# Kernel tuning notes

Measured on AMD Instinct MI355X. Metric: run time of the kernel, lower is better.

## Reference

```python
import jax, jax.numpy as jnp
import numpy as np

EPS = 1e-5
NEG_SLOPE = 0.2

def _bn(x, gamma, beta):
    # BatchNorm1d in training mode: stats over (batch, length) per channel. x: [B,C,N]
    m = jnp.mean(x, axis=(0, 2), keepdims=True)
    v = jnp.mean((x - m) ** 2, axis=(0, 2), keepdims=True)  # biased variance
    return (x - m) * jax.lax.rsqrt(v + EPS) * gamma[None, :, None] + beta[None, :, None]

def setup_inputs() -> dict:
    key = jax.random.key(0)
    ks = jax.random.split(key, 7)
    B, C, N, H = 32, 64, 2048, 128
    s = 1.0 / np.sqrt(C)
    return {
        "x": jax.random.normal(ks[0], (B, C, N), dtype=jnp.float32),
        "wq": jax.random.normal(ks[1], (C, C), dtype=jnp.float32) * s,
        "wk": jax.random.normal(ks[2], (C, C), dtype=jnp.float32) * s,
        "wv": jax.random.normal(ks[3], (C, C), dtype=jnp.float32) * s,
        "w_ff1": jax.random.normal(ks[4], (H, C), dtype=jnp.float32) * s,
        "w_ff2": jax.random.normal(ks[5], (C, H), dtype=jnp.float32) * (1.0 / np.sqrt(H)),
        "bn1_gamma": jnp.ones((C,), dtype=jnp.float32),
        "bn1_beta": jnp.zeros((C,), dtype=jnp.float32),
        "bn2_gamma": jnp.ones((C,), dtype=jnp.float32),
        "bn2_beta": jnp.zeros((C,), dtype=jnp.float32),
    }

def reference(x, wq, wk, wv, w_ff1, w_ff2, bn1_gamma, bn1_beta, bn2_gamma, bn2_beta):
    # x: [B, C, N]; 1x1 convs are per-point channel matmuls
    C = x.shape[1]
    q = jnp.einsum('oc,bcn->bno', wq, x)          # [B,N,C]
    k = jnp.einsum('oc,bcn->bon', wk, x)          # [B,C,N]
    v = jnp.einsum('oc,bcn->bno', wv, x)          # [B,N,C] (v^T)
    energy = jnp.einsum('bnc,bcm->bnm', q, k)     # [B,N,N]
    attention = jax.nn.softmax(energy / jnp.sqrt(jnp.float32(C)), axis=-1)
    x_r = jnp.einsum('bnm,bmc->bcn', attention, v)  # [B,C,N]
    h = _bn(x + x_r, bn1_gamma, bn1_beta)
    ff = jnp.einsum('hc,bcn->bhn', w_ff1, h)      # [B,H,N]
    ff = jnp.where(ff >= 0, ff, NEG_SLOPE * ff)   # LeakyReLU(0.2)
    ff = jnp.einsum('ch,bhn->bcn', w_ff2, ff)     # [B,C,N]
    return _bn(h + ff, bn2_gamma, bn2_beta)
```

## Files before the change

kernel.cpp:

```cpp
#include <hip/hip_runtime.h>

#define B_ 32
#define C_ 64
#define N_ 2048
#define H_ 128

typedef unsigned short u16;
typedef unsigned int u32;
typedef float f32x4 __attribute__((ext_vector_type(4)));
typedef __bf16 bf16x8 __attribute__((ext_vector_type(8)));
typedef __bf16 bf16x4 __attribute__((ext_vector_type(4)));
typedef unsigned short u16x4 __attribute__((ext_vector_type(4)));

#define MFMA(a, b, c) __builtin_amdgcn_mfma_f32_16x16x32_bf16(a, b, c, 0, 0, 0)
#define LOG2E 1.44269504088896f

__device__ __forceinline__ int swz(int row, int cb) { return row * 128 + (cb ^ ((row & 7) << 4)); }
__device__ __forceinline__ int swz256(int row, int cb) { return row * 256 + (cb ^ ((row & 7) << 4)); }

__device__ __forceinline__ float b2f(u16 v) {
    union { u32 u; float f; } x; x.u = ((u32)v) << 16; return x.f;
}

__device__ __forceinline__ bf16x8 cvt8(const float* p, float s) {
    f32x4 a = *(const f32x4*)p, b = *(const f32x4*)(p + 4);
    bf16x8 o;
    o[0] = (__bf16)(a[0] * s); o[1] = (__bf16)(a[1] * s);
    o[2] = (__bf16)(a[2] * s); o[3] = (__bf16)(a[3] * s);
    o[4] = (__bf16)(b[0] * s); o[5] = (__bf16)(b[1] * s);
    o[6] = (__bf16)(b[2] * s); o[7] = (__bf16)(b[3] * s);
    return o;
}

__global__ __launch_bounds__(256) void qkv_k(
    const float* __restrict__ x,
    const float* __restrict__ wq, const float* __restrict__ wk, const float* __restrict__ wv,
    const float* __restrict__ w1, const float* __restrict__ w2,
    u16* __restrict__ Qg, u16* __restrict__ Kg, u16* __restrict__ Vg,
    u16* __restrict__ w1b, u16* __restrict__ w2b)
{
    const int b = blockIdx.y, nt = blockIdx.x, t = threadIdx.x;
    const int lane = t & 63, wave = t >> 6, g = lane >> 4, r16 = lane & 15;
    __shared__ __align__(16) u16 xT[128 * 64];
    const int n0 = nt * 128;

    bf16x8 wqf[4][2], wkf[4][2], wvf[4][2];
#pragma unroll
    for (int jt = 0; jt < 4; ++jt)
#pragma unroll
        for (int kc = 0; kc < 2; ++kc) {
            const int ro = (r16 + 16 * jt) * 64 + 8 * g + 32 * kc;
            wqf[jt][kc] = cvt8(wq + ro, 0.125f * LOG2E);
            wkf[jt][kc] = cvt8(wk + ro, 1.0f);
            wvf[jt][kc] = cvt8(wv + ro, 1.0f);
        }

    {
        int c = t >> 5;
        const int nn = (t & 31) * 4;
#pragma unroll
        for (int pass = 0; pass < 8; ++pass, c += 8) {
            f32x4 v = *(const f32x4*)&x[(size_t)(b * 64 + c) * 2048 + n0 + nn];
#pragma unroll
            for (int j = 0; j < 4; ++j)
                xT[swz(nn + j, 2 * c) >> 1] = __builtin_bit_cast(u16, (__bf16)v[j]);
        }
    }
    if (b == 0 && nt == 0) {
        for (int i = t; i < H_ * C_; i += 256) w1b[i] = __builtin_bit_cast(u16, (__bf16)w1[i]);
        for (int i = t; i < C_ * H_; i += 256) w2b[i] = __builtin_bit_cast(u16, (__bf16)w2[i]);
    }
    __syncthreads();

#pragma unroll
    for (int p = 0; p < 2; ++p) {
        const int nt16 = wave * 2 + p;
        bf16x8 xa[2];
#pragma unroll
        for (int kc = 0; kc < 2; ++kc)
            xa[kc] = *(const bf16x8*)&xT[swz(nt16 * 16 + r16, 16 * g + 64 * kc) >> 1];
#pragma unroll
        for (int jt = 0; jt < 4; ++jt) {
            f32x4 aq = {0.f, 0.f, 0.f, 0.f}, ak = {0.f, 0.f, 0.f, 0.f};
            aq = MFMA(wqf[jt][0], xa[0], aq); aq = MFMA(wqf[jt][1], xa[1], aq);
            ak = MFMA(wkf[jt][0], xa[0], ak); ak = MFMA(wkf[jt][1], xa[1], ak);
            bf16x4 qk, kk;
#pragma unroll
            for (int r = 0; r < 4; ++r) { qk[r] = (__bf16)aq[r]; kk[r] = (__bf16)ak[r]; }
            const size_t ro = (size_t)(b * 2048 + n0 + nt16 * 16 + r16) * 64 + 16 * jt + 4 * g;
            *(bf16x4*)&Qg[ro] = qk;
            *(bf16x4*)&Kg[ro] = kk;
        }
#pragma unroll
        for (int it = 0; it < 4; ++it) {
            f32x4 av = {0.f, 0.f, 0.f, 0.f};
            av = MFMA(xa[0], wvf[it][0], av);
            av = MFMA(xa[1], wvf[it][1], av);
            bf16x4 vk;
#pragma unroll
            for (int r = 0; r < 4; ++r) vk[r] = (__bf16)av[r];
            *(bf16x4*)&Vg[(size_t)(b * 64 + 16 * it + r16) * 2048 + n0 + nt16 * 16 + 4 * g] = vk;
        }
    }
}

__global__ __launch_bounds__(256) void attn_k(
    const u16* __restrict__ Qg, const u16* __restrict__ Kg, const u16* __restrict__ Vg,
    const float* __restrict__ x, u16* __restrict__ yb,
    float* __restrict__ ps, float* __restrict__ pq)
{
    const int t = threadIdx.x;
    const int lane = t & 63, wave = t >> 6, g = lane >> 4, r16 = lane & 15;
    const int L = blockIdx.x;
    const int xcd = L & 7, slot = L >> 3;
    const int b = xcd * 4 + (slot >> 4);
    const int qt = slot & 15;

    __shared__ __align__(16) u16 Lds16[24576];
    char* lds = (char*)Lds16;

    const int n0 = qt * 128 + wave * 32;
    bf16x8 qf[2][2];
#pragma unroll
    for (int u = 0; u < 2; ++u) {
        const u16* qrow = Qg + (size_t)(b * 2048 + n0 + 16 * u + r16) * 64 + 8 * g;
        qf[u][0] = *(const bf16x8*)qrow;
        qf[u][1] = *(const bf16x8*)(qrow + 32);
    }

    f32x4 acc[2][4];
    float m[2] = {-1e30f, -1e30f}, lp[2] = {0.f, 0.f};
#pragma unroll
    for (int u = 0; u < 2; ++u)
#pragma unroll
        for (int ct = 0; ct < 4; ++ct) acc[u][ct] = (f32x4){0.f, 0.f, 0.f, 0.f};

    const char* Kgb = (const char*)Kg + (size_t)b * 2048 * 128;
    const char* Vgb = (const char*)Vg + (size_t)b * 64 * 4096;
    const int srcxor = (((lane & 7) ^ (lane >> 3)) << 4);
    const int rowb = wave * 16 + (lane >> 3);

    int ka[8];
#pragma unroll
    for (int i = 0; i < 8; ++i)
        ka[i] = swz(16 * (i >> 1) + r16, 16 * g + 64 * (i & 1));
    const int pbase = 32768 + wave * 4096;
    int pw[2][4], pr[2][2];
#pragma unroll
    for (int u = 0; u < 2; ++u) {
#pragma unroll
        for (int it = 0; it < 4; ++it) pw[u][it] = pbase + u * 2048 + swz(r16, 32 * it + 8 * g);
#pragma unroll
        for (int kc = 0; kc < 2; ++kc) pr[u][kc] = pbase + u * 2048 + swz(r16, 16 * g + 64 * kc);
    }

    auto stage = [&](int kvt, int buf) {
#pragma unroll
        for (int j = 0; j < 2; ++j) {
            const char* gk = Kgb + (size_t)(kvt * 64 + rowb + 8 * j) * 128 + srcxor;
            const char* gv = Vgb + (size_t)(rowb + 8 * j) * 4096 + kvt * 128 + srcxor;
            char* lk = lds + buf * 8192 + (wave * 2 + j) * 1024;
            __builtin_amdgcn_global_load_lds(
                (const __attribute__((address_space(1))) void*)gk,
                (__attribute__((address_space(3))) void*)lk, 16, 0, 0);
            __builtin_amdgcn_global_load_lds(
                (const __attribute__((address_space(1))) void*)gv,
                (__attribute__((address_space(3))) void*)(lk + 16384), 16, 0, 0);
        }
    };

    auto tile = [&](int kvt, int buf) {
        __syncthreads();
        if (kvt + 1 < 32) stage(kvt + 1, buf ^ 1);
        const char* Kc = lds + buf * 8192;
        const char* Vc = Kc + 16384;

        bf16x8 kf[8];
#pragma unroll
        for (int i = 0; i < 8; ++i) kf[i] = *(const bf16x8*)(Kc + ka[i]);
        f32x4 s[2][4];
        __builtin_amdgcn_s_setprio(1);
#pragma unroll
        for (int it = 0; it < 4; ++it) {
            f32x4 a0 = {0.f, 0.f, 0.f, 0.f}, a1 = {0.f, 0.f, 0.f, 0.f};
            a0 = MFMA(kf[2 * it], qf[0][0], a0); a0 = MFMA(kf[2 * it + 1], qf[0][1], a0);
            a1 = MFMA(kf[2 * it], qf[1][0], a1); a1 = MFMA(kf[2 * it + 1], qf[1][1], a1);
            s[0][it] = a0; s[1][it] = a1;
        }
        __builtin_amdgcn_s_setprio(0);
        bf16x8 vf[8];
#pragma unroll
        for (int i = 0; i < 8; ++i) vf[i] = *(const bf16x8*)(Vc + ka[i]);

#pragma unroll
        for (int u = 0; u < 2; ++u) {
            float mi[4];
#pragma unroll
            for (int it = 0; it < 4; ++it)
                mi[it] = fmaxf(fmaxf(s[u][it][0], s[u][it][1]),
                               fmaxf(s[u][it][2], s[u][it][3]));
            float pm = fmaxf(fmaxf(mi[0], mi[1]), fmaxf(mi[2], mi[3]));
            pm = fmaxf(pm, __shfl_xor(pm, 16, 64));
            pm = fmaxf(pm, __shfl_xor(pm, 32, 64));
            if (!__all(pm <= m[u] + 8.f)) {
                const float mn = fmaxf(m[u], pm);
                const float al = exp2f(m[u] - mn);
                m[u] = mn; lp[u] *= al;
#pragma unroll
                for (int ct = 0; ct < 4; ++ct)
#pragma unroll
                    for (int r = 0; r < 4; ++r) acc[u][ct][r] *= al;
            }
            float ts[4];
#pragma unroll
            for (int it = 0; it < 4; ++it) {
                const float p0 = exp2f(s[u][it][0] - m[u]);
                const float p1 = exp2f(s[u][it][1] - m[u]);
                const float p2 = exp2f(s[u][it][2] - m[u]);
                const float p3 = exp2f(s[u][it][3] - m[u]);
                ts[it] = (p0 + p1) + (p2 + p3);
                bf16x4 pk;
                pk[0] = (__bf16)p0; pk[1] = (__bf16)p1;
                pk[2] = (__bf16)p2; pk[3] = (__bf16)p3;
                *(bf16x4*)(lds + pw[u][it]) = pk;
            }
            lp[u] += (ts[0] + ts[1]) + (ts[2] + ts[3]);
        }
        bf16x8 pf[2][2];
#pragma unroll
        for (int u = 0; u < 2; ++u) {
            pf[u][0] = *(const bf16x8*)(lds + pr[u][0]);
            pf[u][1] = *(const bf16x8*)(lds + pr[u][1]);
        }
        __builtin_amdgcn_s_setprio(1);
#pragma unroll
        for (int u = 0; u < 2; ++u)
#pragma unroll
            for (int ct = 0; ct < 4; ++ct) {
                acc[u][ct] = MFMA(vf[2 * ct], pf[u][0], acc[u][ct]);
                acc[u][ct] = MFMA(vf[2 * ct + 1], pf[u][1], acc[u][ct]);
            }
        __builtin_amdgcn_s_setprio(0);
    };

    stage(0, 0);
#pragma unroll 1
    for (int kvt = 0; kvt < 32; kvt += 2) {
        tile(kvt, 0);
        tile(kvt + 1, 1);
    }

    float sv[4][4], qv[4][4];
#pragma unroll
    for (int ct = 0; ct < 4; ++ct)
#pragma unroll
        for (int r = 0; r < 4; ++r) { sv[ct][r] = 0.f; qv[ct][r] = 0.f; }
#pragma unroll
    for (int u = 0; u < 2; ++u) {
        float l = lp[u];
        l += __shfl_xor(l, 16, 64);
        l += __shfl_xor(l, 32, 64);
        const float inv = 1.0f / l;
        const int n = n0 + 16 * u + r16;
#pragma unroll
        for (int ct = 0; ct < 4; ++ct) {
            bf16x4 ov;
#pragma unroll
            for (int r = 0; r < 4; ++r) {
                const int c = 16 * ct + 4 * g + r;
                const float o = acc[u][ct][r] * inv + x[(size_t)(b * 64 + c) * 2048 + n];
                sv[ct][r] += o;
                qv[ct][r] += o * o;
                ov[r] = (__bf16)o;
            }
            *(bf16x4*)&yb[(size_t)(b * 2048 + n) * 64 + 16 * ct + 4 * g] = ov;
        }
    }
#pragma unroll
    for (int d = 1; d <= 8; d <<= 1)
#pragma unroll
        for (int ct = 0; ct < 4; ++ct)
#pragma unroll
            for (int r = 0; r < 4; ++r) {
                sv[ct][r] += __shfl_xor(sv[ct][r], d, 64);
                qv[ct][r] += __shfl_xor(qv[ct][r], d, 64);
            }
    __syncthreads();
    float* sb = (float*)(lds + 32768);
    if (r16 == 0) {
#pragma unroll
        for (int ct = 0; ct < 4; ++ct)
#pragma unroll
            for (int r = 0; r < 4; ++r) {
                const int c = 16 * ct + 4 * g + r;
                sb[wave * 64 + c] = sv[ct][r];
                sb[256 + wave * 64 + c] = qv[ct][r];
            }
    }
    __syncthreads();
    if (t < 64) {
        ps[L * 64 + t] = sb[t] + sb[64 + t] + sb[128 + t] + sb[192 + t];
        pq[L * 64 + t] = sb[256 + t] + sb[320 + t] + sb[384 + t] + sb[448 + t];
    }
}

__global__ __launch_bounds__(256) void finalize_k(
    const float* __restrict__ psum, const float* __restrict__ psq,
    const float* __restrict__ gamma, const float* __restrict__ beta,
    float* __restrict__ ss, int nblk)
{
    const int c = blockIdx.x, t = threadIdx.x;
    const int lane = t & 63, wave = t >> 6;
    float s = 0.f, q = 0.f;
    for (int bl = t; bl < nblk; bl += 256) {
        s += psum[bl * 64 + c];
        q += psq[bl * 64 + c];
    }
#pragma unroll
    for (int d = 1; d <= 32; d <<= 1) {
        s += __shfl_xor(s, d, 64);
        q += __shfl_xor(q, d, 64);
    }
    __shared__ float ls[4], lq[4];
    if (lane == 0) { ls[wave] = s; lq[wave] = q; }
    __syncthreads();
    if (t == 0) {
        s = ls[0] + ls[1] + ls[2] + ls[3];
        q = lq[0] + lq[1] + lq[2] + lq[3];
        const float mean = s * (1.0f / 65536.0f);
        const float var  = q * (1.0f / 65536.0f) - mean * mean;
        const float sc   = rsqrtf(var + 1e-5f) * gamma[c];
        ss[c] = sc;
        ss[64 + c] = beta[c] - mean * sc;
    }
}

__global__ __launch_bounds__(256) void ff_k(
    const u16* __restrict__ y, const float* __restrict__ ss1,
    const u16* __restrict__ w1b, const u16* __restrict__ w2b,
    u16* __restrict__ zb, float* __restrict__ ps, float* __restrict__ pq)
{
    const int b = blockIdx.y, nt = blockIdx.x, t = threadIdx.x;
    const int lane = t & 63, wave = t >> 6, g = lane >> 4, r16 = lane & 15;
    const int L = blockIdx.y * gridDim.x + blockIdx.x;
    __shared__ __align__(16) u16 hT[64 * 64];
    __shared__ __align__(16) float hf[64 * 68];
    __shared__ __align__(16) u16 pb[4][16 * 128];
    __shared__ float sc1[64], sh1[64];
    if (t < 64) { sc1[t] = ss1[t]; sh1[t] = ss1[64 + t]; }
    __syncthreads();
    const int n0 = nt * 64;
    {
        const int i = t >> 2, c0 = (t & 3) * 16;
        u16 yb16[16] __attribute__((aligned(16)));
        *(uint4*)&yb16[0] = *(const uint4*)&y[(size_t)(b * 2048 + n0 + i) * 64 + c0];
        *(uint4*)&yb16[8] = *(const uint4*)&y[(size_t)(b * 2048 + n0 + i) * 64 + c0 + 8];
        u16 hb[16] __attribute__((aligned(16)));
#pragma unroll
        for (int j = 0; j < 16; ++j) {
            const int c = c0 + j;
            const float hv = b2f(yb16[j]) * sc1[c] + sh1[c];
            hf[i * 68 + c] = hv;
            hb[j] = __builtin_bit_cast(u16, (__bf16)hv);
        }
        *(uint4*)&hT[swz(i, 2 * c0) >> 1]      = *(const uint4*)&hb[0];
        *(uint4*)&hT[swz(i, 2 * c0 + 16) >> 1] = *(const uint4*)&hb[8];
    }
    __syncthreads();

    bf16x8 ha[2];
#pragma unroll
    for (int kc = 0; kc < 2; ++kc)
        ha[kc] = *(const bf16x8*)&hT[swz(wave * 16 + r16, 16 * g + 64 * kc) >> 1];
#pragma unroll
    for (int it = 0; it < 8; ++it) {
        f32x4 a = {0.f, 0.f, 0.f, 0.f};
#pragma unroll
        for (int kc = 0; kc < 2; ++kc) {
            bf16x8 w1f = *(const bf16x8*)&w1b[(r16 + 16 * it) * 64 + 8 * g + 32 * kc];
            a = MFMA(w1f, ha[kc], a);
        }
        u16x4 pk;
#pragma unroll
        for (int r = 0; r < 4; ++r) {
            const float rv = a[r] >= 0.f ? a[r] : 0.2f * a[r];
            pk[r] = __builtin_bit_cast(u16, (__bf16)rv);
        }
        *(u16x4*)&pb[wave][swz256(r16, 2 * (16 * it + 4 * g)) >> 1] = pk;
    }
    bf16x8 pa[4];
#pragma unroll
    for (int kc = 0; kc < 4; ++kc)
        pa[kc] = *(const bf16x8*)&pb[wave][swz256(r16, 16 * g + 64 * kc) >> 1];
    const int nl = wave * 16 + r16;
    float sv[4][4], qv[4][4];
#pragma unroll
    for (int jt = 0; jt < 4; ++jt) {
        f32x4 a = {0.f, 0.f, 0.f, 0.f};
#pragma unroll
        for (int kc = 0; kc < 4; ++kc) {
            bf16x8 w2f = *(const bf16x8*)&w2b[(r16 + 16 * jt) * 128 + 8 * g + 32 * kc];
            a = MFMA(w2f, pa[kc], a);
        }
        f32x4 h4 = *(const f32x4*)&hf[nl * 68 + 16 * jt + 4 * g];
        bf16x4 zk;
#pragma unroll
        for (int r = 0; r < 4; ++r) {
            a[r] += h4[r];
            sv[jt][r] = a[r];
            qv[jt][r] = a[r] * a[r];
            zk[r] = (__bf16)a[r];
        }
        *(bf16x4*)&zb[(size_t)(b * 2048 + n0 + nl) * 64 + 16 * jt + 4 * g] = zk;
    }
#pragma unroll
    for (int d = 1; d <= 8; d <<= 1)
#pragma unroll
        for (int jt = 0; jt < 4; ++jt)
#pragma unroll
            for (int r = 0; r < 4; ++r) {
                sv[jt][r] += __shfl_xor(sv[jt][r], d, 64);
                qv[jt][r] += __shfl_xor(qv[jt][r], d, 64);
            }
    __syncthreads();
    float* sb = (float*)&pb[0][0];
    if (r16 == 0) {
#pragma unroll
        for (int jt = 0; jt < 4; ++jt)
#pragma unroll
            for (int r = 0; r < 4; ++r) {
                const int c = 16 * jt + 4 * g + r;
                sb[wave * 64 + c] = sv[jt][r];
                sb[256 + wave * 64 + c] = qv[jt][r];
            }
    }
    __syncthreads();
    if (t < 64) {
        ps[L * 64 + t] = sb[t] + sb[64 + t] + sb[128 + t] + sb[192 + t];
        pq[L * 64 + t] = sb[256 + t] + sb[320 + t] + sb[384 + t] + sb[448 + t];
    }
}

__global__ __launch_bounds__(256) void bnout_k(
    const u16* __restrict__ zb, const float* __restrict__ ss2, float* __restrict__ out)
{
    const int b = blockIdx.y, nt = blockIdx.x, t = threadIdx.x;
    __shared__ float tile[64 * 65];
    __shared__ float sc2[64], sh2[64];
    if (t < 64) { sc2[t] = ss2[t]; sh2[t] = ss2[64 + t]; }
    __syncthreads();
    const int n0 = nt * 64;
    {
        const int i = t >> 2, c0 = (t & 3) * 16;
        u16 zb16[16] __attribute__((aligned(16)));
        *(uint4*)&zb16[0] = *(const uint4*)&zb[(size_t)(b * 2048 + n0 + i) * 64 + c0];
        *(uint4*)&zb16[8] = *(const uint4*)&zb[(size_t)(b * 2048 + n0 + i) * 64 + c0 + 8];
#pragma unroll
        for (int j = 0; j < 16; ++j) {
            const int c = c0 + j;
            tile[i * 65 + c] = b2f(zb16[j]) * sc2[c] + sh2[c];
        }
    }
    __syncthreads();
    {
        const int c = t >> 2, j0 = (t & 3) * 16;
#pragma unroll
        for (int q4 = 0; q4 < 4; ++q4) {
            f32x4 ov;
#pragma unroll
            for (int j = 0; j < 4; ++j)
                ov[j] = tile[(j0 + 4 * q4 + j) * 65 + c];
            *(f32x4*)&out[(size_t)(b * 64 + c) * 2048 + n0 + j0 + 4 * q4] = ov;
        }
    }
}

extern "C" void kernel_launch(void* const* d_in, const int* in_sizes, int n_in,
                              void* d_out, int out_size, void* d_ws, size_t ws_size,
                              hipStream_t stream)
{
    const float* x   = (const float*)d_in[0];
    const float* wq  = (const float*)d_in[1];
    const float* wk  = (const float*)d_in[2];
    const float* wv  = (const float*)d_in[3];
    const float* w1  = (const float*)d_in[4];
    const float* w2  = (const float*)d_in[5];
    const float* g1  = (const float*)d_in[6];
    const float* be1 = (const float*)d_in[7];
    const float* g2  = (const float*)d_in[8];
    const float* be2 = (const float*)d_in[9];
    float* out = (float*)d_out;

    char* w = (char*)d_ws;
    u16* Qg = (u16*)w;   w += (size_t)B_ * N_ * C_ * 2;
    u16* Kg = (u16*)w;   w += (size_t)B_ * N_ * C_ * 2;
    u16* Vg = (u16*)w;   w += (size_t)B_ * N_ * C_ * 2;
    u16* yb = (u16*)w;   w += (size_t)B_ * N_ * C_ * 2;
    u16* zb = (u16*)w;   w += (size_t)B_ * N_ * C_ * 2;
    u16* w1b = (u16*)w;  w += (size_t)H_ * C_ * 2;
    u16* w2b = (u16*)w;  w += (size_t)C_ * H_ * 2;
    float* ps1 = (float*)w; w += 1024 * 64 * 4;
    float* pq1 = (float*)w; w += 1024 * 64 * 4;
    float* ps2 = (float*)w; w += 1024 * 64 * 4;
    float* pq2 = (float*)w; w += 1024 * 64 * 4;
    float* ss1 = (float*)w; w += 128 * 4;
    float* ss2 = (float*)w; w += 128 * 4;

    const dim3 blk(256);
    hipLaunchKernelGGL(qkv_k,   dim3(16, 32), blk, 0, stream, x, wq, wk, wv, w1, w2, Qg, Kg, Vg, w1b, w2b);
    hipLaunchKernelGGL(attn_k,  dim3(512),    blk, 0, stream, Qg, Kg, Vg, x, yb, ps1, pq1);
    hipLaunchKernelGGL(finalize_k, dim3(64),  blk, 0, stream, ps1, pq1, g1, be1, ss1, 512);
    hipLaunchKernelGGL(ff_k,    dim3(32, 32), blk, 0, stream, yb, ss1, w1b, w2b, zb, ps2, pq2);
    hipLaunchKernelGGL(finalize_k, dim3(64),  blk, 0, stream, ps2, pq2, g2, be2, ss2, 1024);
    hipLaunchKernelGGL(bnout_k, dim3(32, 32), blk, 0, stream, zb, ss2, out);
}
```

Baseline: 144.9 us.

## Switch attention to 32x32x16 MFMA and pass P in registers via permlane swap

```diff
diff --git a/kernel.cpp b/kernel.cpp
--- a/kernel.cpp
+++ b/kernel.cpp
@@ -8,11 +8,15 @@
 typedef unsigned short u16;
 typedef unsigned int u32;
 typedef float f32x4 __attribute__((ext_vector_type(4)));
+typedef float f32x16 __attribute__((ext_vector_type(16)));
 typedef __bf16 bf16x8 __attribute__((ext_vector_type(8)));
 typedef __bf16 bf16x4 __attribute__((ext_vector_type(4)));
 typedef unsigned short u16x4 __attribute__((ext_vector_type(4)));
+typedef unsigned int u32x4v __attribute__((ext_vector_type(4)));
 
 #define MFMA(a, b, c) __builtin_amdgcn_mfma_f32_16x16x32_bf16(a, b, c, 0, 0, 0)
+#define MFMA32(a, b, c) __builtin_amdgcn_mfma_f32_32x32x16_bf16(a, b, c, 0, 0, 0)
+#define EXP2(x) __builtin_amdgcn_exp2f(x)
 #define LOG2E 1.44269504088896f
 
 __device__ __forceinline__ int swz(int row, int cb) { return row * 128 + (cb ^ ((row & 7) << 4)); }
@@ -20,6 +24,22 @@
 
 __device__ __forceinline__ float b2f(u16 v) {
     union { u32 u; float f; } x; x.u = ((u32)v) << 16; return x.f;
+}
+
+__device__ __forceinline__ u32 cvtpk(float lo, float hi) {
+    u32 r;
+    asm("v_cvt_pk_bf16_f32 %0, %1, %2" : "=v"(r) : "v"(lo), "v"(hi));
+    return r;
+}
+
+__device__ __forceinline__ bf16x8 pfrag(float p0, float p1, float p2, float p3,
+                                        float p4, float p5, float p6, float p7) {
+    u32 x1 = cvtpk(p0, p1), x2 = cvtpk(p2, p3);
+    u32 y1 = cvtpk(p4, p5), y2 = cvtpk(p6, p7);
+    asm volatile("v_permlane32_swap_b32 %0, %1" : "+v"(x1), "+v"(y1));
+    asm volatile("v_permlane32_swap_b32 %0, %1" : "+v"(x2), "+v"(y2));
+    u32x4v d; d[0] = x1; d[1] = x2; d[2] = y1; d[3] = y2;
+    return __builtin_bit_cast(bf16x8, d);
 }
 
 __device__ __forceinline__ bf16x8 cvt8(const float* p, float s) {
@@ -110,49 +130,37 @@
     float* __restrict__ ps, float* __restrict__ pq)
 {
     const int t = threadIdx.x;
-    const int lane = t & 63, wave = t >> 6, g = lane >> 4, r16 = lane & 15;
+    const int lane = t & 63, wave = t >> 6, q = lane & 31, hi = lane >> 5;
     const int L = blockIdx.x;
     const int xcd = L & 7, slot = L >> 3;
     const int b = xcd * 4 + (slot >> 4);
     const int qt = slot & 15;
 
-    __shared__ __align__(16) u16 Lds16[24576];
+    __shared__ __align__(16) u16 Lds16[16384];
     char* lds = (char*)Lds16;
 
     const int n0 = qt * 128 + wave * 32;
-    bf16x8 qf[2][2];
-#pragma unroll
-    for (int u = 0; u < 2; ++u) {
-        const u16* qrow = Qg + (size_t)(b * 2048 + n0 + 16 * u + r16) * 64 + 8 * g;
-        qf[u][0] = *(const bf16x8*)qrow;
-        qf[u][1] = *(const bf16x8*)(qrow + 32);
-    }
-
-    f32x4 acc[2][4];
-    float m[2] = {-1e30f, -1e30f}, lp[2] = {0.f, 0.f};
-#pragma unroll
-    for (int u = 0; u < 2; ++u)
-#pragma unroll
-        for (int ct = 0; ct < 4; ++ct) acc[u][ct] = (f32x4){0.f, 0.f, 0.f, 0.f};
+    const int n = n0 + q;
+
+    bf16x8 qf[4];
+    {
+        const u16* qrow = Qg + (size_t)(b * 2048 + n) * 64 + 8 * hi;
+#pragma unroll
+        for (int kc = 0; kc < 4; ++kc)
+            qf[kc] = *(const bf16x8*)(qrow + 16 * kc);
+    }
+
+    f32x16 acc[2];
+#pragma unroll
+    for (int ct = 0; ct < 2; ++ct)
+#pragma unroll
+        for (int r = 0; r < 16; ++r) acc[ct][r] = 0.f;
+    float m = -1e30f, lp = 0.f;
 
     const char* Kgb = (const char*)Kg + (size_t)b * 2048 * 128;
     const char* Vgb = (const char*)Vg + (size_t)b * 64 * 4096;
     const int srcxor = (((lane & 7) ^ (lane >> 3)) << 4);
     const int rowb = wave * 16 + (lane >> 3);
-
-    int ka[8];
-#pragma unroll
-    for (int i = 0; i < 8; ++i)
-        ka[i] = swz(16 * (i >> 1) + r16, 16 * g + 64 * (i & 1));
-    const int pbase = 32768 + wave * 4096;
-    int pw[2][4], pr[2][2];
-#pragma unroll
-    for (int u = 0; u < 2; ++u) {
-#pragma unroll
-        for (int it = 0; it < 4; ++it) pw[u][it] = pbase + u * 2048 + swz(r16, 32 * it + 8 * g);
-#pragma unroll
-        for (int kc = 0; kc < 2; ++kc) pr[u][kc] = pbase + u * 2048 + swz(r16, 16 * g + 64 * kc);
-    }
 
     auto stage = [&](int kvt, int buf) {
 #pragma unroll
@@ -175,71 +183,77 @@
         const char* Kc = lds + buf * 8192;
         const char* Vc = Kc + 16384;
 
-        bf16x8 kf[8];
-#pragma unroll
-        for (int i = 0; i < 8; ++i) kf[i] = *(const bf16x8*)(Kc + ka[i]);
-        f32x4 s[2][4];
+        f32x16 st[2];
         __builtin_amdgcn_s_setprio(1);
 #pragma unroll
-        for (int it = 0; it < 4; ++it) {
-            f32x4 a0 = {0.f, 0.f, 0.f, 0.f}, a1 = {0.f, 0.f, 0.f, 0.f};
-            a0 = MFMA(kf[2 * it], qf[0][0], a0); a0 = MFMA(kf[2 * it + 1], qf[0][1], a0);
-            a1 = MFMA(kf[2 * it], qf[1][0], a1); a1 = MFMA(kf[2 * it + 1], qf[1][1], a1);
-            s[0][it] = a0; s[1][it] = a1;
+        for (int it = 0; it < 2; ++it) {
+            f32x16 a;
+#pragma unroll
+            for (int r = 0; r < 16; ++r) a[r] = 0.f;
+#pragma unroll
+            for (int kc = 0; kc < 4; ++kc) {
+                bf16x8 kf = *(const bf16x8*)(Kc + swz(32 * it + q, 32 * kc + 16 * hi));
+                a = MFMA32(kf, qf[kc], a);
+            }
+            st[it] = a;
         }
         __builtin_amdgcn_s_setprio(0);
-        bf16x8 vf[8];
-#pragma unroll
-        for (int i = 0; i < 8; ++i) vf[i] = *(const bf16x8*)(Vc + ka[i]);
-
-#pragma unroll
-        for (int u = 0; u < 2; ++u) {
-            float mi[4];
-#pragma unroll
-            for (int it = 0; it < 4; ++it)
-                mi[it] = fmaxf(fmaxf(s[u][it][0], s[u][it][1]),
-                               fmaxf(s[u][it][2], s[u][it][3]));
-            float pm = fmaxf(fmaxf(mi[0], mi[1]), fmaxf(mi[2], mi[3]));
-            pm = fmaxf(pm, __shfl_xor(pm, 16, 64));
-            pm = fmaxf(pm, __shfl_xor(pm, 32, 64));
-            if (!__all(pm <= m[u] + 8.f)) {
-                const float mn = fmaxf(m[u], pm);
-                const float al = exp2f(m[u] - mn);
-                m[u] = mn; lp[u] *= al;
-#pragma unroll
-                for (int ct = 0; ct < 4; ++ct)
-#pragma unroll
-                    for (int r = 0; r < 4; ++r) acc[u][ct][r] *= al;
-            }
-            float ts[4];
-#pragma unroll
-            for (int it = 0; it < 4; ++it) {
-                const float p0 = exp2f(s[u][it][0] - m[u]);
-                const float p1 = exp2f(s[u][it][1] - m[u]);
-                const float p2 = exp2f(s[u][it][2] - m[u]);
-                const float p3 = exp2f(s[u][it][3] - m[u]);
-                ts[it] = (p0 + p1) + (p2 + p3);
-                bf16x4 pk;
-                pk[0] = (__bf16)p0; pk[1] = (__bf16)p1;
-                pk[2] = (__bf16)p2; pk[3] = (__bf16)p3;
-                *(bf16x4*)(lds + pw[u][it]) = pk;
-            }
-            lp[u] += (ts[0] + ts[1]) + (ts[2] + ts[3]);
-        }
-        bf16x8 pf[2][2];
-#pragma unroll
-        for (int u = 0; u < 2; ++u) {
-            pf[u][0] = *(const bf16x8*)(lds + pr[u][0]);
-            pf[u][1] = *(const bf16x8*)(lds + pr[u][1]);
-        }
+
+        bf16x8 vf[2][4];
+#pragma unroll
+        for (int ct = 0; ct < 2; ++ct)
+#pragma unroll
+            for (int mc = 0; mc < 4; ++mc)
+                vf[ct][mc] = *(const bf16x8*)(Vc + swz(32 * ct + q, 32 * mc + 16 * hi));
+
+        float mx[2];
+#pragma unroll
+        for (int it = 0; it < 2; ++it) {
+            float a0 = fmaxf(fmaxf(st[it][0], st[it][1]), fmaxf(st[it][2], st[it][3]));
+            float a1 = fmaxf(fmaxf(st[it][4], st[it][5]), fmaxf(st[it][6], st[it][7]));
+            float a2 = fmaxf(fmaxf(st[it][8], st[it][9]), fmaxf(st[it][10], st[it][11]));
+            float a3 = fmaxf(fmaxf(st[it][12], st[it][13]), fmaxf(st[it][14], st[it][15]));
+            mx[it] = fmaxf(fmaxf(a0, a1), fmaxf(a2, a3));
+        }
+        float pm = fmaxf(mx[0], mx[1]);
+        pm = fmaxf(pm, __shfl_xor(pm, 32, 64));
+        if (!__all(pm <= m + 8.f)) {
+            const float mn = fmaxf(m, pm);
+            const float al = EXP2(m - mn);
+            m = mn; lp *= al;
+#pragma unroll
+            for (int ct = 0; ct < 2; ++ct)
+#pragma unroll
+                for (int r = 0; r < 16; ++r) acc[ct][r] *= al;
+        }
+        float ls = 0.f;
+#pragma unroll
+        for (int it = 0; it < 2; ++it) {
+#pragma unroll
+            for (int r = 0; r < 16; ++r) st[it][r] = EXP2(st[it][r] - m);
+            float a0 = (st[it][0] + st[it][1]) + (st[it][2] + st[it][3]);
+            float a1 = (st[it][4] + st[it][5]) + (st[it][6] + st[it][7]);
+            float a2 = (st[it][8] + st[it][9]) + (st[it][10] + st[it][11]);
+            float a3 = (st[it][12] + st[it][13]) + (st[it][14] + st[it][15]);
+            ls += (a0 + a1) + (a2 + a3);
+        }
+        lp += ls;
+        bf16x8 pf0 = pfrag(st[0][0], st[0][1], st[0][2], st[0][3],
+                           st[0][4], st[0][5], st[0][6], st[0][7]);
+        bf16x8 pf1 = pfrag(st[0][8], st[0][9], st[0][10], st[0][11],
+                           st[0][12], st[0][13], st[0][14], st[0][15]);
+        bf16x8 pf2 = pfrag(st[1][0], st[1][1], st[1][2], st[1][3],
+                           st[1][4], st[1][5], st[1][6], st[1][7]);
+        bf16x8 pf3 = pfrag(st[1][8], st[1][9], st[1][10], st[1][11],
+                           st[1][12], st[1][13], st[1][14], st[1][15]);
         __builtin_amdgcn_s_setprio(1);
 #pragma unroll
-        for (int u = 0; u < 2; ++u)
-#pragma unroll
-            for (int ct = 0; ct < 4; ++ct) {
-                acc[u][ct] = MFMA(vf[2 * ct], pf[u][0], acc[u][ct]);
-                acc[u][ct] = MFMA(vf[2 * ct + 1], pf[u][1], acc[u][ct]);
-            }
+        for (int ct = 0; ct < 2; ++ct) {
+            acc[ct] = MFMA32(vf[ct][0], pf0, acc[ct]);
+            acc[ct] = MFMA32(vf[ct][1], pf1, acc[ct]);
+            acc[ct] = MFMA32(vf[ct][2], pf2, acc[ct]);
+            acc[ct] = MFMA32(vf[ct][3], pf3, acc[ct]);
+        }
         __builtin_amdgcn_s_setprio(0);
     };
 
@@ -250,49 +264,44 @@
         tile(kvt + 1, 1);
     }
 
-    float sv[4][4], qv[4][4];
-#pragma unroll
-    for (int ct = 0; ct < 4; ++ct)
-#pragma unroll
-        for (int r = 0; r < 4; ++r) { sv[ct][r] = 0.f; qv[ct][r] = 0.f; }
-#pragma unroll
-    for (int u = 0; u < 2; ++u) {
-        float l = lp[u];
-        l += __shfl_xor(l, 16, 64);
-        l += __shfl_xor(l, 32, 64);
-        const float inv = 1.0f / l;
-        const int n = n0 + 16 * u + r16;
-#pragma unroll
-        for (int ct = 0; ct < 4; ++ct) {
+    const float l = lp + __shfl_xor(lp, 32, 64);
+    const float inv = 1.0f / l;
+    float sv[2][16], qv[2][16];
+#pragma unroll
+    for (int ct = 0; ct < 2; ++ct)
+#pragma unroll
+        for (int r = 0; r < 16; ++r) {
+            const int c = 32 * ct + (r & 3) + 8 * (r >> 2) + 4 * hi;
+            const float o = acc[ct][r] * inv + x[(size_t)(b * 64 + c) * 2048 + n];
+            sv[ct][r] = o;
+            qv[ct][r] = o * o;
+        }
+#pragma unroll
+    for (int ct = 0; ct < 2; ++ct)
+#pragma unroll
+        for (int grp = 0; grp < 4; ++grp) {
             bf16x4 ov;
 #pragma unroll
-            for (int r = 0; r < 4; ++r) {
-                const int c = 16 * ct + 4 * g + r;
-                const float o = acc[u][ct][r] * inv + x[(size_t)(b * 64 + c) * 2048 + n];
-                sv[ct][r] += o;
-                qv[ct][r] += o * o;
-                ov[r] = (__bf16)o;
-            }
-            *(bf16x4*)&yb[(size_t)(b * 2048 + n) * 64 + 16 * ct + 4 * g] = ov;
-        }
-    }
-#pragma unroll
-    for (int d = 1; d <= 8; d <<= 1)
-#pragma unroll
-        for (int ct = 0; ct < 4; ++ct)
-#pragma unroll
-            for (int r = 0; r < 4; ++r) {
+            for (int r = 0; r < 4; ++r) ov[r] = (__bf16)sv[ct][4 * grp + r];
+            *(bf16x4*)&yb[(size_t)(b * 2048 + n) * 64 + 32 * ct + 8 * grp + 4 * hi] = ov;
+        }
+#pragma unroll
+    for (int d = 1; d <= 16; d <<= 1)
+#pragma unroll
+        for (int ct = 0; ct < 2; ++ct)
+#pragma unroll
+            for (int r = 0; r < 16; ++r) {
                 sv[ct][r] += __shfl_xor(sv[ct][r], d, 64);
                 qv[ct][r] += __shfl_xor(qv[ct][r], d, 64);
             }
     __syncthreads();
-    float* sb = (float*)(lds + 32768);
-    if (r16 == 0) {
-#pragma unroll
-        for (int ct = 0; ct < 4; ++ct)
-#pragma unroll
-            for (int r = 0; r < 4; ++r) {
-                const int c = 16 * ct + 4 * g + r;
+    float* sb = (float*)lds;
+    if (q == 0) {
+#pragma unroll
+        for (int ct = 0; ct < 2; ++ct)
+#pragma unroll
+            for (int r = 0; r < 16; ++r) {
+                const int c = 32 * ct + (r & 3) + 8 * (r >> 2) + 4 * hi;
                 sb[wave * 64 + c] = sv[ct][r];
                 sb[256 + wave * 64 + c] = qv[ct][r];
             }
```

After: 127.5 us. -12.0%, faster.
